# Performance work log

Measured on AMD Instinct MI355X. Metric: run time of the kernel, lower is better.

The kernel has to match this reference:

```python
import jax, jax.numpy as jnp
import numpy as np

I = 512   # input_size
H = 512   # hidden_size
Z = 0.1   # zoneout rate (eval-mode deterministic blend)
S = 128   # number of segments
B = 64    # batch


def setup_inputs() -> dict:
    rng = np.random.default_rng(0)
    durs = rng.integers(4, 13, size=(S, B)).astype(np.int64)  # [S, B], all >= 1
    T = int(durs.sum(0).max())
    key = jax.random.key(0)
    k0, k1, k2, k3, k4 = jax.random.split(key, 5)
    k = 1.0 / np.sqrt(H)
    x = jax.random.normal(k0, (T, B, I), jnp.float32)
    W_ih = jax.random.uniform(k1, (4 * H, I), jnp.float32, -k, k)
    W_hh = jax.random.uniform(k2, (4 * H, H), jnp.float32, -k, k)
    b_ih = jax.random.uniform(k3, (4 * H,), jnp.float32, -k, k)
    b_hh = jax.random.uniform(k4, (4 * H,), jnp.float32, -k, k)
    return {"x": x, "durs": jnp.asarray(durs), "W_ih": W_ih, "W_hh": W_hh,
            "b_ih": b_ih, "b_hh": b_hh}


def _duration_masks(durs, T):
    # durs: [S, B] -> per-batch segment-end (reset) frame indices and masks
    durs_bs = durs.T                                   # [B, S]
    reset_idx = jnp.cumsum(durs_bs, axis=1) - 1        # [B, S] last frame of each segment
    mel_lengths = jnp.sum(durs_bs, axis=1)             # [B]
    t = jnp.arange(T)
    reset_mask = jnp.any(t[None, :, None] == reset_idx[:, None, :], axis=-1)  # [B, T]
    valid = t[None, :] < mel_lengths[:, None]          # [B, T] frames within mel length
    retain = (~reset_mask) & valid                     # state kept where not reset/pad
    return reset_idx, retain.T, valid.T                # retain/valid as [T, B]


def reference(x, durs, W_ih, W_hh, b_ih, b_hh):
    T, Bb, _ = x.shape
    reset_idx, retain, valid = _duration_masks(durs, T)
    # Precompute the input contribution to the gates for all timesteps (one big GEMM)
    xg = jnp.einsum('tbi,gi->tbg', x, W_ih) + b_ih + b_hh   # [T, B, 4H]
    retain_f = retain.astype(x.dtype)                       # [T, B]

    def step(carry, inp):
        h, c = carry
        xg_t, retain_t = inp
        gates = xg_t + h @ W_hh.T                           # [B, 4H]
        i, f, g, o = jnp.split(gates, 4, axis=-1)           # torch LSTMCell order i,f,g,o
        i = jax.nn.sigmoid(i); f = jax.nn.sigmoid(f); o = jax.nn.sigmoid(o)
        g = jnp.tanh(g)
        c_new = f * c + i * g
        h_new = o * jnp.tanh(c_new)
        # eval-mode zoneout: deterministic blend with previous state
        h_z = Z * h + (1.0 - Z) * h_new
        c_z = Z * c + (1.0 - Z) * c_new
        m = retain_t[:, None]                               # zero state at segment resets / padding
        return (h_z * m, c_z * m), h_z

    h0 = jnp.zeros((Bb, H), x.dtype)
    (h, c), outputs = jax.lax.scan(step, (h0, h0), (xg, retain_f))
    outputs = outputs * valid[:, :, None].astype(outputs.dtype)  # [T, B, H]
    # segout: hidden state at each segment's last frame -> [B, S, H]
    segout = jnp.take_along_axis(outputs.transpose(1, 0, 2), reset_idx[:, :, None], axis=1)
    return outputs, h, c, segout
```

## Files before the change

### kernel.cpp

```cpp
#include <hip/hip_runtime.h>
#include <hip/hip_fp16.h>

#define IDIM 512
#define HDIM 512
#define NGATE 2048
#define SEGS 128
#define BATCH 64
#define ZK 0.1f

typedef _Float16 f16;
typedef _Float16 f16x8 __attribute__((ext_vector_type(8)));
typedef float f32x4 __attribute__((ext_vector_type(4)));

__device__ __forceinline__ void gload16(const void* g, void* l) {
  __builtin_amdgcn_global_load_lds((const __attribute__((address_space(1))) void*)g,
                                   (__attribute__((address_space(3))) void*)l, 16, 0, 0);
}
__device__ __forceinline__ float sigmoidf_(float x) { return 1.0f / (1.0f + __expf(-x)); }
__device__ __forceinline__ float tanhf_(float x) { return 2.0f / (1.0f + __expf(-2.0f * x)) - 1.0f; }

__global__ void prep_kernel(const int* __restrict__ durs, int4* __restrict__ meta,
                            int* __restrict__ Mk, int* __restrict__ mel) {
  __shared__ int hist[16];
  __shared__ int cur[16];
  int tid = threadIdx.x;
  if (tid < 16) hist[tid] = 0;
  __syncthreads();
  int b = tid;
  for (int s = 0; s < SEGS; ++s) {
    int d = durs[s * BATCH + b] & 15;
    atomicAdd(&hist[d], 1);
  }
  __syncthreads();
  if (tid == 0) {
    int run = 0;
    for (int d = 15; d >= 0; --d) { cur[d] = run; run += hist[d]; }
    for (int kk = 0; kk < 12; ++kk) Mk[kk] = cur[kk];
  }
  __syncthreads();
  int run = 0;
  for (int s = 0; s < SEGS; ++s) {
    int d = durs[s * BATCH + b] & 15;
    int pos = atomicAdd(&cur[d], 1);
    meta[pos] = make_int4(run, b, s, d);
    run += d;
  }
  mel[b] = run;
}

__global__ void wprep_kernel(const float* __restrict__ Wih, const float* __restrict__ Whh,
                             const float* __restrict__ bih, const float* __restrict__ bhh,
                             f16* __restrict__ Wc, float* __restrict__ biasp) {
  int n = blockIdx.x;
  int G = n >> 6, q = (n >> 4) & 3, r = n & 15;
  int j = G * 16 + r;
  int orig = q * 512 + j;
  for (int kk = threadIdx.x; kk < 1024; kk += blockDim.x) {
    float v = (kk < 512) ? Wih[(size_t)orig * 512 + kk] : Whh[(size_t)orig * 512 + kk - 512];
    Wc[(size_t)n * 1024 + kk] = (f16)v;
  }
  if (threadIdx.x == 0) biasp[n] = bih[orig] + bhh[orig];
}

__global__ void xconv_kernel(const float* __restrict__ x, f16* __restrict__ xh, long n8) {
  long i = (long)blockIdx.x * blockDim.x + threadIdx.x;
  long stride = (long)gridDim.x * blockDim.x;
  for (; i < n8; i += stride) {
    const float4* p = (const float4*)(x + i * 8);
    float4 a = p[0], bv = p[1];
    f16x8 o;
    o[0] = (f16)a.x;  o[1] = (f16)a.y;  o[2] = (f16)a.z;  o[3] = (f16)a.w;
    o[4] = (f16)bv.x; o[5] = (f16)bv.y; o[6] = (f16)bv.z; o[7] = (f16)bv.w;
    *(f16x8*)(xh + i * 8) = o;
  }
}

__global__ void zero_kernel(float* __restrict__ out, const int* __restrict__ mel, int T) {
  int bid = blockIdx.x;
  int tb = T * BATCH;
  if (bid < tb) {
    int t = bid / BATCH, b = bid - t * BATCH;
    if (t < mel[b]) return;
    float4* p = (float4*)(out + (size_t)bid * HDIM);
    p[threadIdx.x] = make_float4(0.f, 0.f, 0.f, 0.f);
  } else {
    int e = bid - tb;
    float4* p = (float4*)(out + (size_t)tb * HDIM + (size_t)e * HDIM);
    p[threadIdx.x] = make_float4(0.f, 0.f, 0.f, 0.f);
  }
}

template <bool FIRST>
__global__ __launch_bounds__(512, 1)
void step256_kernel(const f16* __restrict__ xh, const f16* __restrict__ Wc,
                    const float* __restrict__ biasp,
                    const f16* __restrict__ hprev, f16* __restrict__ hnext,
                    float* __restrict__ cst,
                    const int4* __restrict__ meta, const int* __restrict__ Mk,
                    float* __restrict__ out, int T, int k) {
  const int mk = Mk[k];
  const int nbx = gridDim.x;
  const int nwg = nbx * gridDim.y;
  const int orig = blockIdx.y * nbx + blockIdx.x;
  const int cpx = nwg >> 3;
  const int swz = (orig & 7) * cpx + (orig >> 3);
  const int by = swz / nbx, bx = swz - by * nbx;
  const int m0 = by * 256;
  if (m0 >= mk) return;
  const int n0 = bx * 256;

  __shared__ __align__(16) f16 As[2][256][64];
  __shared__ __align__(16) f16 Bs[2][256][64];
  __shared__ int4 metaS[256];

  const int tid = threadIdx.x;
  const int lane = tid & 63;
  const int w = tid >> 6;
  const int wr = w >> 2;
  const int wc = w & 3;
  const int lr = lane & 15;
  const int lk = lane >> 4;

  if (tid < 256) metaS[tid] = meta[m0 + tid];

  const int swzc = (((lane & 7) ^ ((lane >> 3) & 7)) << 3);
  size_t xoff[4];
  int ra4[4];
#pragma unroll
  for (int o = 0; o < 4; ++o) {
    int trow = o * 64 + w * 8 + (lane >> 3);
    int r = m0 + trow;
    int ra = (r < mk) ? r : 0;
    int4 mt = meta[ra];
    xoff[o] = ((size_t)(mt.x + k) * BATCH + mt.y) * IDIM + swzc;
    ra4[o] = ra;
  }

  auto stageA = [&](int o, int kb, int slot) {
    const f16* src;
    if (FIRST || kb < 8) src = xh + xoff[o] + kb * 64;
    else src = hprev + (size_t)ra4[o] * HDIM + (kb - 8) * 64 + swzc;
    gload16(src, &As[slot][o * 64 + w * 8][0]);
  };
  auto stageB = [&](int o, int kb, int slot) {
    int trow = o * 64 + w * 8 + (lane >> 3);
    gload16(Wc + (size_t)(n0 + trow) * 1024 + (size_t)kb * 64 + swzc,
            &Bs[slot][o * 64 + w * 8][0]);
  };

  auto lda = [&](int slot, int h, int f, int ks) -> f16x8 {
    int row = wr * 128 + h * 64 + f * 16 + lr;
    int ch = (((ks * 4 + lk) ^ (lr & 7)) << 3);
    return *(const f16x8*)&As[slot][row][ch];
  };
  auto ldb = [&](int slot, int q, int ks) -> f16x8 {
    int row = wc * 64 + q * 16 + lr;
    int ch = (((ks * 4 + lk) ^ (lr & 7)) << 3);
    return *(const f16x8*)&Bs[slot][row][ch];
  };

  f32x4 acc[8][4];
#pragma unroll
  for (int a = 0; a < 8; ++a)
#pragma unroll
    for (int bb = 0; bb < 4; ++bb) acc[a][bb] = (f32x4){0.f, 0.f, 0.f, 0.f};

  const int KB = FIRST ? 8 : 16;

#pragma unroll
  for (int o = 0; o < 4; ++o) stageA(o, 0, 0);
#pragma unroll
  for (int o = 0; o < 4; ++o) stageB(o, 0, 0);
#pragma unroll
  for (int o = 0; o < 4; ++o) stageA(o, 1, 1);
#pragma unroll
  for (int o = 0; o < 4; ++o) stageB(o, 1, 1);
  asm volatile("s_waitcnt vmcnt(8)" ::: "memory");
  __builtin_amdgcn_s_barrier();

  f16x8 aF[4][2], bF[4][2];

  for (int kt = 0; kt < KB; ++kt) {
    const int s = kt & 1;
    const bool st1 = (kt + 1 < KB);
    const bool st2 = (kt + 2 < KB);

#pragma unroll
    for (int f = 0; f < 4; ++f)
#pragma unroll
      for (int ks = 0; ks < 2; ++ks) aF[f][ks] = lda(s, 0, f, ks);
#pragma unroll
    for (int q = 0; q < 4; ++q)
#pragma unroll
      for (int ks = 0; ks < 2; ++ks) bF[q][ks] = ldb(s, q, ks);
    __builtin_amdgcn_s_barrier();
    __builtin_amdgcn_s_setprio(1);
#pragma unroll
    for (int f = 0; f < 4; ++f)
#pragma unroll
      for (int fn = 0; fn < 2; ++fn)
#pragma unroll
        for (int ks = 0; ks < 2; ++ks)
          acc[f][fn] = __builtin_amdgcn_mfma_f32_16x16x32_f16(aF[f][ks], bF[fn][ks], acc[f][fn], 0, 0, 0);
    __builtin_amdgcn_s_setprio(0);
    __builtin_amdgcn_s_barrier();

    if (st2) {
#pragma unroll
      for (int o = 0; o < 4; ++o) stageB(o, kt + 2, s);
    }
    __builtin_amdgcn_s_barrier();
    __builtin_amdgcn_s_setprio(1);
#pragma unroll
    for (int f = 0; f < 4; ++f)
#pragma unroll
      for (int fn = 2; fn < 4; ++fn)
#pragma unroll
        for (int ks = 0; ks < 2; ++ks)
          acc[f][fn] = __builtin_amdgcn_mfma_f32_16x16x32_f16(aF[f][ks], bF[fn][ks], acc[f][fn], 0, 0, 0);
    __builtin_amdgcn_s_setprio(0);
    __builtin_amdgcn_s_barrier();

#pragma unroll
    for (int f = 0; f < 4; ++f)
#pragma unroll
      for (int ks = 0; ks < 2; ++ks) aF[f][ks] = lda(s, 1, f, ks);
    if (st2) { stageA(0, kt + 2, s); stageA(2, kt + 2, s); }
    __builtin_amdgcn_s_barrier();
    __builtin_amdgcn_s_setprio(1);
#pragma unroll
    for (int f = 0; f < 4; ++f)
#pragma unroll
      for (int fn = 0; fn < 2; ++fn)
#pragma unroll
        for (int ks = 0; ks < 2; ++ks)
          acc[4 + f][fn] = __builtin_amdgcn_mfma_f32_16x16x32_f16(aF[f][ks], bF[fn][ks], acc[4 + f][fn], 0, 0, 0);
    __builtin_amdgcn_s_setprio(0);
    __builtin_amdgcn_s_barrier();

    if (st2) { stageA(1, kt + 2, s); stageA(3, kt + 2, s); }
    __builtin_amdgcn_s_setprio(1);
#pragma unroll
    for (int f = 0; f < 4; ++f)
#pragma unroll
      for (int fn = 2; fn < 4; ++fn)
#pragma unroll
        for (int ks = 0; ks < 2; ++ks)
          acc[4 + f][fn] = __builtin_amdgcn_mfma_f32_16x16x32_f16(aF[f][ks], bF[fn][ks], acc[4 + f][fn], 0, 0, 0);
    __builtin_amdgcn_s_setprio(0);
    if (st2) {
      asm volatile("s_waitcnt vmcnt(8)" ::: "memory");
    } else if (st1) {
      asm volatile("s_waitcnt vmcnt(0)" ::: "memory");
    }
    __builtin_amdgcn_s_barrier();
  }

  float bq[4];
#pragma unroll
  for (int q = 0; q < 4; ++q) bq[q] = biasp[n0 + wc * 64 + q * 16 + lr];
  const int j = ((n0 + wc * 64) >> 6) * 16 + lr;
  const size_t segoff = (size_t)T * BATCH * HDIM + (size_t)2 * BATCH * HDIM;

#pragma unroll
  for (int fm = 0; fm < 8; ++fm) {
#pragma unroll
    for (int reg = 0; reg < 4; ++reg) {
      int m = m0 + wr * 128 + fm * 16 + ((lane >> 4) << 2) + reg;
      if (m >= mk) continue;
      int4 mt = metaS[m - m0];
      float gi = acc[fm][0][reg] + bq[0];
      float gf = acc[fm][1][reg] + bq[1];
      float gg = acc[fm][2][reg] + bq[2];
      float go = acc[fm][3][reg] + bq[3];
      float iv = sigmoidf_(gi), fv = sigmoidf_(gf);
      float gv = tanhf_(gg), ov = sigmoidf_(go);
      float cp, hp;
      if (FIRST) { cp = 0.f; hp = 0.f; }
      else {
        cp = cst[(size_t)m * HDIM + j];
        hp = (float)hprev[(size_t)m * HDIM + j];
      }
      float cn = fv * cp + iv * gv;
      float hn = ov * tanhf_(cn);
      float hz = ZK * hp + (1.f - ZK) * hn;
      float cz = ZK * cp + (1.f - ZK) * cn;
      out[((size_t)(mt.x + k) * BATCH + mt.y) * HDIM + j] = hz;
      if (k == mt.w - 1) {
        out[segoff + ((size_t)mt.y * SEGS + mt.z) * HDIM + j] = hz;
      } else {
        hnext[(size_t)m * HDIM + j] = (f16)hz;
        cst[(size_t)m * HDIM + j] = cz;
      }
    }
  }
}

template <bool FIRST>
__global__ void step_kernel(const f16* __restrict__ xh, const f16* __restrict__ Wc,
                            const float* __restrict__ biasp,
                            const f16* __restrict__ hprev, f16* __restrict__ hnext,
                            float* __restrict__ cst,
                            const int4* __restrict__ meta, const int* __restrict__ Mk,
                            float* __restrict__ out, int T, int k) {
  const int mk = Mk[k];
  const int m0 = blockIdx.y * 128;
  if (m0 >= mk) return;
  const int n0 = blockIdx.x * 128;

  __shared__ __align__(16) f16 At[128][64];
  __shared__ __align__(16) f16 Bt[128][64];
  __shared__ int4 metaS[128];

  const int tid = threadIdx.x;
  const int lane = tid & 63;
  const int w = tid >> 6;
  const int wr = w >> 1, wc = w & 1;

  if (tid < 128) metaS[tid] = meta[m0 + tid];

  const f16* xsrc[4];
  const f16* hsrc[4];
  const f16* wsrc[4];
#pragma unroll
  for (int i = 0; i < 4; ++i) {
    int r = m0 + w * 32 + i * 8 + (lane >> 3);
    int ra = (r < mk) ? r : 0;
    int4 mt = meta[ra];
    xsrc[i] = xh + ((size_t)(mt.x + k) * BATCH + mt.y) * IDIM;
    hsrc[i] = hprev + (size_t)ra * HDIM;
    wsrc[i] = Wc + (size_t)(n0 + w * 32 + i * 8 + (lane >> 3)) * 1024;
  }
  const int koff = (lane & 7) * 8;

  f32x4 acc[4][4];
#pragma unroll
  for (int a = 0; a < 4; ++a)
#pragma unroll
    for (int bb = 0; bb < 4; ++bb) acc[a][bb] = (f32x4){0.f, 0.f, 0.f, 0.f};

  const int KB = FIRST ? 8 : 16;
  for (int kb = 0; kb < KB; ++kb) {
    __syncthreads();
#pragma unroll
    for (int i = 0; i < 4; ++i) {
      const f16* s;
      if (FIRST) s = xsrc[i] + kb * 64 + koff;
      else       s = (kb < 8) ? (xsrc[i] + kb * 64 + koff) : (hsrc[i] + (kb - 8) * 64 + koff);
      gload16(s, &At[w * 32 + i * 8][0]);
    }
#pragma unroll
    for (int i = 0; i < 4; ++i) gload16(wsrc[i] + kb * 64 + koff, &Bt[w * 32 + i * 8][0]);
    __syncthreads();

    const int lr = lane & 15;
    const int lk = (lane >> 4) * 8;
#pragma unroll
    for (int ks = 0; ks < 2; ++ks) {
      f16x8 af[4], bfr[4];
#pragma unroll
      for (int f = 0; f < 4; ++f) af[f] = *(const f16x8*)&At[wr * 64 + f * 16 + lr][ks * 32 + lk];
#pragma unroll
      for (int f = 0; f < 4; ++f) bfr[f] = *(const f16x8*)&Bt[wc * 64 + f * 16 + lr][ks * 32 + lk];
#pragma unroll
      for (int fm = 0; fm < 4; ++fm)
#pragma unroll
        for (int fn = 0; fn < 4; ++fn)
          acc[fm][fn] = __builtin_amdgcn_mfma_f32_16x16x32_f16(af[fm], bfr[fn], acc[fm][fn], 0, 0, 0);
    }
  }

  const int r15 = lane & 15;
  float bq[4];
#pragma unroll
  for (int q = 0; q < 4; ++q) bq[q] = biasp[n0 + wc * 64 + q * 16 + r15];
  const int j = ((n0 + wc * 64) >> 6) * 16 + r15;
  const size_t segoff = (size_t)T * BATCH * HDIM + (size_t)2 * BATCH * HDIM;

#pragma unroll
  for (int fm = 0; fm < 4; ++fm) {
#pragma unroll
    for (int reg = 0; reg < 4; ++reg) {
      int m = m0 + wr * 64 + fm * 16 + ((lane >> 4) << 2) + reg;
      if (m >= mk) continue;
      int4 mt = metaS[m - m0];
      float gi = acc[fm][0][reg] + bq[0];
      float gf = acc[fm][1][reg] + bq[1];
      float gg = acc[fm][2][reg] + bq[2];
      float go = acc[fm][3][reg] + bq[3];
      float iv = sigmoidf_(gi), fv = sigmoidf_(gf);
      float gv = tanhf_(gg), ov = sigmoidf_(go);
      float cp, hp;
      if (FIRST) { cp = 0.f; hp = 0.f; }
      else {
        cp = cst[(size_t)m * HDIM + j];
        hp = (float)hprev[(size_t)m * HDIM + j];
      }
      float cn = fv * cp + iv * gv;
      float hn = ov * tanhf_(cn);
      float hz = ZK * hp + (1.f - ZK) * hn;
      float cz = ZK * cp + (1.f - ZK) * cn;
      out[((size_t)(mt.x + k) * BATCH + mt.y) * HDIM + j] = hz;
      if (k == mt.w - 1) {
        out[segoff + ((size_t)mt.y * SEGS + mt.z) * HDIM + j] = hz;
      } else {
        hnext[(size_t)m * HDIM + j] = (f16)hz;
        cst[(size_t)m * HDIM + j] = cz;
      }
    }
  }
}

extern "C" void kernel_launch(void* const* d_in, const int* in_sizes, int n_in,
                              void* d_out, int out_size, void* d_ws, size_t ws_size,
                              hipStream_t stream) {
  const float* x = (const float*)d_in[0];
  const int* durs = (const int*)d_in[1];
  const float* Wih = (const float*)d_in[2];
  const float* Whh = (const float*)d_in[3];
  const float* bih = (const float*)d_in[4];
  const float* bhh = (const float*)d_in[5];
  float* out = (float*)d_out;
  const int T = in_sizes[0] / (BATCH * IDIM);

  char* ws = (char*)d_ws;
  size_t off = 0;
  auto alloc = [&](size_t bytes) {
    void* p = ws + off;
    off = (off + bytes + 255) & ~(size_t)255;
    return p;
  };
  f16* xh     = (f16*)alloc((size_t)T * BATCH * IDIM * 2);
  f16* Wc     = (f16*)alloc((size_t)NGATE * 1024 * 2);
  float* biasp= (float*)alloc((size_t)NGATE * 4);
  f16* hst0   = (f16*)alloc((size_t)SEGS * BATCH * HDIM * 2);
  f16* hst1   = (f16*)alloc((size_t)SEGS * BATCH * HDIM * 2);
  float* cst  = (float*)alloc((size_t)SEGS * BATCH * HDIM * 4);
  int4* meta  = (int4*)alloc((size_t)SEGS * BATCH * 16);
  int* Mk     = (int*)alloc(64);
  int* mel    = (int*)alloc(64);

  prep_kernel<<<1, 64, 0, stream>>>(durs, meta, Mk, mel);
  wprep_kernel<<<NGATE, 256, 0, stream>>>(Wih, Whh, bih, bhh, Wc, biasp);
  long n8 = (long)T * BATCH * IDIM / 8;
  xconv_kernel<<<2048, 256, 0, stream>>>(x, xh, n8);
  zero_kernel<<<T * BATCH + 128, 128, 0, stream>>>(out, mel, T);

  dim3 hgrid(8, 32);
  step256_kernel<true><<<hgrid, 512, 0, stream>>>(xh, Wc, biasp, hst0, hst1, cst, meta, Mk, out, T, 0);
  for (int k = 1; k < 8; ++k) {
    f16* hp = (k & 1) ? hst1 : hst0;
    f16* hn = (k & 1) ? hst0 : hst1;
    step256_kernel<false><<<hgrid, 512, 0, stream>>>(xh, Wc, biasp, hp, hn, cst, meta, Mk, out, T, k);
  }
  dim3 sgrid(16, 64);
  for (int k = 8; k < 12; ++k) {
    f16* hp = (k & 1) ? hst1 : hst0;
    f16* hn = (k & 1) ? hst0 : hst1;
    step_kernel<false><<<sgrid, 256, 0, stream>>>(xh, Wc, biasp, hp, hn, cst, meta, Mk, out, T, k);
  }
}
```

Before: 654.7 us.

## Hoist input projection into one batched GEMM ahead of the recurrent steps

Splits the combined [x,h] weight into separate input and recurrent halves. All input-gate products for every active row and step are computed up front in one large GEMM, gathered through a row map and stored in fp16 with the bias folded in. Each recurrent step then does only the K=512 hidden-state GEMM and adds the precomputed gates in the epilogue, and step 0 becomes a pure elementwise kernel. The costs are a large fp16 intermediate buffer, an extra write and read of it, and fp16 rounding of the pre-activation gates. The zero kernel becomes grid-strided.

```diff
diff --git a/kernel.cpp b/kernel.cpp
--- a/kernel.cpp
+++ b/kernel.cpp
@@ -7,6 +7,7 @@
 #define SEGS 128
 #define BATCH 64
 #define ZK 0.1f
+#define XGROWS 98304
 
 typedef _Float16 f16;
 typedef _Float16 f16x8 __attribute__((ext_vector_type(8)));
@@ -27,15 +28,14 @@
   if (tid < 16) hist[tid] = 0;
   __syncthreads();
   int b = tid;
-  for (int s = 0; s < SEGS; ++s) {
-    int d = durs[s * BATCH + b] & 15;
-    atomicAdd(&hist[d], 1);
-  }
+  for (int s = 0; s < SEGS; ++s) atomicAdd(&hist[durs[s * BATCH + b] & 15], 1);
   __syncthreads();
   if (tid == 0) {
     int run = 0;
     for (int d = 15; d >= 0; --d) { cur[d] = run; run += hist[d]; }
-    for (int kk = 0; kk < 12; ++kk) Mk[kk] = cur[kk];
+    int off = 0;
+    for (int kk = 0; kk < 12; ++kk) { Mk[kk] = cur[kk]; Mk[12 + kk] = off; off += cur[kk]; }
+    Mk[24] = off;
   }
   __syncthreads();
   int run = 0;
@@ -48,16 +48,30 @@
   mel[b] = run;
 }
 
+__global__ void zrowmap_kernel(int* __restrict__ rowmap) {
+  rowmap[blockIdx.x * 256 + threadIdx.x] = 0;
+}
+
+__global__ void rowmap_kernel(const int4* __restrict__ meta, const int* __restrict__ Mk,
+                              int* __restrict__ rowmap) {
+  int k = blockIdx.y;
+  int m = blockIdx.x * 256 + threadIdx.x;
+  if (m < Mk[k]) {
+    int4 mt = meta[m];
+    rowmap[Mk[12 + k] + m] = (mt.x + k) * BATCH + mt.y;
+  }
+}
+
 __global__ void wprep_kernel(const float* __restrict__ Wih, const float* __restrict__ Whh,
                              const float* __restrict__ bih, const float* __restrict__ bhh,
-                             f16* __restrict__ Wc, float* __restrict__ biasp) {
+                             f16* __restrict__ Wihp, f16* __restrict__ Whhp,
+                             float* __restrict__ biasp) {
   int n = blockIdx.x;
   int G = n >> 6, q = (n >> 4) & 3, r = n & 15;
-  int j = G * 16 + r;
-  int orig = q * 512 + j;
-  for (int kk = threadIdx.x; kk < 1024; kk += blockDim.x) {
-    float v = (kk < 512) ? Wih[(size_t)orig * 512 + kk] : Whh[(size_t)orig * 512 + kk - 512];
-    Wc[(size_t)n * 1024 + kk] = (f16)v;
+  int orig = q * 512 + G * 16 + r;
+  for (int kk = threadIdx.x; kk < 512; kk += blockDim.x) {
+    Wihp[(size_t)n * 512 + kk] = (f16)Wih[(size_t)orig * 512 + kk];
+    Whhp[(size_t)n * 512 + kk] = (f16)Whh[(size_t)orig * 512 + kk];
   }
   if (threadIdx.x == 0) biasp[n] = bih[orig] + bhh[orig];
 }
@@ -75,30 +89,225 @@
   }
 }
 
-__global__ void zero_kernel(float* __restrict__ out, const int* __restrict__ mel, int T) {
-  int bid = blockIdx.x;
+__global__ void zero_kernel(float* __restrict__ out, const int* __restrict__ mel,
+                            int T, int total) {
   int tb = T * BATCH;
-  if (bid < tb) {
-    int t = bid / BATCH, b = bid - t * BATCH;
-    if (t < mel[b]) return;
-    float4* p = (float4*)(out + (size_t)bid * HDIM);
-    p[threadIdx.x] = make_float4(0.f, 0.f, 0.f, 0.f);
-  } else {
-    int e = bid - tb;
-    float4* p = (float4*)(out + (size_t)tb * HDIM + (size_t)e * HDIM);
-    p[threadIdx.x] = make_float4(0.f, 0.f, 0.f, 0.f);
-  }
-}
-
-template <bool FIRST>
+  for (int bid = blockIdx.x; bid < total; bid += gridDim.x) {
+    if (bid < tb) {
+      int t = bid / BATCH, b = bid - t * BATCH;
+      if (t < mel[b]) continue;
+      float4* p = (float4*)(out + (size_t)bid * HDIM);
+      p[threadIdx.x] = make_float4(0.f, 0.f, 0.f, 0.f);
+    } else {
+      int e = bid - tb;
+      float4* p = (float4*)(out + (size_t)tb * HDIM + (size_t)e * HDIM);
+      p[threadIdx.x] = make_float4(0.f, 0.f, 0.f, 0.f);
+    }
+  }
+}
+
 __global__ __launch_bounds__(512, 1)
-void step256_kernel(const f16* __restrict__ xh, const f16* __restrict__ Wc,
-                    const float* __restrict__ biasp,
+void xg_gemm_kernel(const f16* __restrict__ xh, const f16* __restrict__ Wihp,
+                    const float* __restrict__ biasp, const int* __restrict__ rowmap,
+                    const int* __restrict__ Mk, f16* __restrict__ xg) {
+  const int orig = blockIdx.y * 8 + blockIdx.x;
+  const int swz = (orig & 7) * 384 + (orig >> 3);
+  const int by = swz >> 3, bx = swz & 7;
+  const int r0 = by * 256;
+  if (r0 >= Mk[24]) return;
+  const int n0 = bx * 256;
+
+  __shared__ __align__(16) f16 SM[65536];
+  f16 (*As)[256][64] = (f16(*)[256][64])SM;
+  f16 (*Bs)[256][64] = (f16(*)[256][64])(SM + 32768);
+
+  const int tid = threadIdx.x;
+  const int lane = tid & 63;
+  const int w = tid >> 6;
+  const int wr = w >> 2;
+  const int wc = w & 3;
+  const int lr = lane & 15;
+  const int lk = lane >> 4;
+
+  const int swzc = (((lane & 7) ^ ((lane >> 3) & 7)) << 3);
+  const f16* asrc[4];
+  const f16* wsrc[4];
+#pragma unroll
+  for (int o = 0; o < 4; ++o) {
+    int trow = o * 64 + w * 8 + (lane >> 3);
+    asrc[o] = xh + (size_t)rowmap[r0 + trow] * IDIM + swzc;
+    wsrc[o] = Wihp + (size_t)(n0 + trow) * 512 + swzc;
+  }
+
+  auto stageA = [&](int o, int kb, int slot) {
+    gload16(asrc[o] + kb * 64, &As[slot][o * 64 + w * 8][0]);
+  };
+  auto stageB = [&](int o, int kb, int slot) {
+    gload16(wsrc[o] + kb * 64, &Bs[slot][o * 64 + w * 8][0]);
+  };
+  auto lda = [&](int slot, int h, int f, int ks) -> f16x8 {
+    int row = wr * 128 + h * 64 + f * 16 + lr;
+    int ch = (((ks * 4 + lk) ^ (lr & 7)) << 3);
+    return *(const f16x8*)&As[slot][row][ch];
+  };
+  auto ldb = [&](int slot, int q, int ks) -> f16x8 {
+    int row = wc * 64 + q * 16 + lr;
+    int ch = (((ks * 4 + lk) ^ (lr & 7)) << 3);
+    return *(const f16x8*)&Bs[slot][row][ch];
+  };
+
+  f32x4 acc[8][4];
+#pragma unroll
+  for (int a = 0; a < 8; ++a)
+#pragma unroll
+    for (int bb = 0; bb < 4; ++bb) acc[a][bb] = (f32x4){0.f, 0.f, 0.f, 0.f};
+
+  const int KB = 8;
+#pragma unroll
+  for (int o = 0; o < 4; ++o) stageA(o, 0, 0);
+#pragma unroll
+  for (int o = 0; o < 4; ++o) stageB(o, 0, 0);
+#pragma unroll
+  for (int o = 0; o < 4; ++o) stageA(o, 1, 1);
+#pragma unroll
+  for (int o = 0; o < 4; ++o) stageB(o, 1, 1);
+  asm volatile("s_waitcnt vmcnt(8)" ::: "memory");
+  __builtin_amdgcn_s_barrier();
+
+  f16x8 aF[4][2], bF[4][2];
+  for (int kt = 0; kt < KB; ++kt) {
+    const int s = kt & 1;
+    const bool st1 = (kt + 1 < KB);
+    const bool st2 = (kt + 2 < KB);
+
+#pragma unroll
+    for (int f = 0; f < 4; ++f)
+#pragma unroll
+      for (int ks = 0; ks < 2; ++ks) aF[f][ks] = lda(s, 0, f, ks);
+#pragma unroll
+    for (int q = 0; q < 4; ++q)
+#pragma unroll
+      for (int ks = 0; ks < 2; ++ks) bF[q][ks] = ldb(s, q, ks);
+    __builtin_amdgcn_s_barrier();
+    __builtin_amdgcn_s_setprio(1);
+#pragma unroll
+    for (int f = 0; f < 4; ++f)
+#pragma unroll
+      for (int fn = 0; fn < 2; ++fn)
+#pragma unroll
+        for (int ks = 0; ks < 2; ++ks)
+          acc[f][fn] = __builtin_amdgcn_mfma_f32_16x16x32_f16(aF[f][ks], bF[fn][ks], acc[f][fn], 0, 0, 0);
+    __builtin_amdgcn_s_setprio(0);
+    __builtin_amdgcn_s_barrier();
+
+    if (st2) {
+#pragma unroll
+      for (int o = 0; o < 4; ++o) stageB(o, kt + 2, s);
+    }
+    __builtin_amdgcn_s_barrier();
+    __builtin_amdgcn_s_setprio(1);
+#pragma unroll
+    for (int f = 0; f < 4; ++f)
+#pragma unroll
+      for (int fn = 2; fn < 4; ++fn)
+#pragma unroll
+        for (int ks = 0; ks < 2; ++ks)
+          acc[f][fn] = __builtin_amdgcn_mfma_f32_16x16x32_f16(aF[f][ks], bF[fn][ks], acc[f][fn], 0, 0, 0);
+    __builtin_amdgcn_s_setprio(0);
+    __builtin_amdgcn_s_barrier();
+
+#pragma unroll
+    for (int f = 0; f < 4; ++f)
+#pragma unroll
+      for (int ks = 0; ks < 2; ++ks) aF[f][ks] = lda(s, 1, f, ks);
+    if (st2) { stageA(0, kt + 2, s); stageA(2, kt + 2, s); }
+    __builtin_amdgcn_s_barrier();
+    __builtin_amdgcn_s_setprio(1);
+#pragma unroll
+    for (int f = 0; f < 4; ++f)
+#pragma unroll
+      for (int fn = 0; fn < 2; ++fn)
+#pragma unroll
+        for (int ks = 0; ks < 2; ++ks)
+          acc[4 + f][fn] = __builtin_amdgcn_mfma_f32_16x16x32_f16(aF[f][ks], bF[fn][ks], acc[4 + f][fn], 0, 0, 0);
+    __builtin_amdgcn_s_setprio(0);
+    __builtin_amdgcn_s_barrier();
+
+    if (st2) { stageA(1, kt + 2, s); stageA(3, kt + 2, s); }
+    __builtin_amdgcn_s_setprio(1);
+#pragma unroll
+    for (int f = 0; f < 4; ++f)
+#pragma unroll
+      for (int fn = 2; fn < 4; ++fn)
+#pragma unroll
+        for (int ks = 0; ks < 2; ++ks)
+          acc[4 + f][fn] = __builtin_amdgcn_mfma_f32_16x16x32_f16(aF[f][ks], bF[fn][ks], acc[4 + f][fn], 0, 0, 0);
+    __builtin_amdgcn_s_setprio(0);
+    if (st2) {
+      asm volatile("s_waitcnt vmcnt(8)" ::: "memory");
+    } else if (st1) {
+      asm volatile("s_waitcnt vmcnt(0)" ::: "memory");
+    }
+    __builtin_amdgcn_s_barrier();
+  }
+
+  float bq[4];
+#pragma unroll
+  for (int q = 0; q < 4; ++q) bq[q] = biasp[n0 + wc * 64 + q * 16 + lr];
+  __syncthreads();
+  f16* SM2 = SM;
+#pragma unroll
+  for (int fm = 0; fm < 8; ++fm)
+#pragma unroll
+    for (int reg = 0; reg < 4; ++reg) {
+      int lm = wr * 128 + fm * 16 + ((lane >> 4) << 2) + reg;
+#pragma unroll
+      for (int q = 0; q < 4; ++q)
+        SM2[lm * 256 + wc * 64 + q * 16 + lr] = (f16)(acc[fm][q][reg] + bq[q]);
+    }
+  __syncthreads();
+#pragma unroll
+  for (int i = 0; i < 16; ++i) {
+    int idx = i * 512 + tid;
+    int lm = idx >> 5, c = idx & 31;
+    *(f16x8*)(xg + ((size_t)(r0 + lm) * NGATE + n0 + c * 8)) =
+        *(const f16x8*)&SM2[lm * 256 + c * 8];
+  }
+}
+
+__global__ void step0_kernel(const f16* __restrict__ xg, const int4* __restrict__ meta,
+                             f16* __restrict__ hnext, float* __restrict__ cst,
+                             float* __restrict__ out) {
+  __shared__ f16 xr[NGATE];
+  int m = blockIdx.x;
+  int tid = threadIdx.x;
+  *(f16x8*)&xr[tid * 8] = *(const f16x8*)&xg[(size_t)m * NGATE + tid * 8];
+  __syncthreads();
+  int4 mt = meta[m];
+#pragma unroll
+  for (int u = 0; u < 2; ++u) {
+    int jj = tid * 2 + u;
+    int base = (jj >> 4) * 64 + (jj & 15);
+    float iv = sigmoidf_((float)xr[base]);
+    float gv = tanhf_((float)xr[base + 32]);
+    float ov = sigmoidf_((float)xr[base + 48]);
+    float cn = iv * gv;
+    float hn = ov * tanhf_(cn);
+    float hz = (1.f - ZK) * hn, cz = (1.f - ZK) * cn;
+    out[((size_t)mt.x * BATCH + mt.y) * HDIM + jj] = hz;
+    hnext[(size_t)m * HDIM + jj] = (f16)hz;
+    cst[(size_t)m * HDIM + jj] = cz;
+  }
+}
+
+__global__ __launch_bounds__(512, 1)
+void step256_kernel(const f16* __restrict__ xg, const f16* __restrict__ Whhp,
                     const f16* __restrict__ hprev, f16* __restrict__ hnext,
                     float* __restrict__ cst,
                     const int4* __restrict__ meta, const int* __restrict__ Mk,
                     float* __restrict__ out, int T, int k) {
   const int mk = Mk[k];
+  const int offk = Mk[12 + k];
   const int nbx = gridDim.x;
   const int nwg = nbx * gridDim.y;
   const int orig = blockIdx.y * nbx + blockIdx.x;
@@ -124,30 +333,23 @@
   if (tid < 256) metaS[tid] = meta[m0 + tid];
 
   const int swzc = (((lane & 7) ^ ((lane >> 3) & 7)) << 3);
-  size_t xoff[4];
-  int ra4[4];
+  const f16* asrc[4];
+  const f16* wsrc[4];
 #pragma unroll
   for (int o = 0; o < 4; ++o) {
     int trow = o * 64 + w * 8 + (lane >> 3);
     int r = m0 + trow;
     int ra = (r < mk) ? r : 0;
-    int4 mt = meta[ra];
-    xoff[o] = ((size_t)(mt.x + k) * BATCH + mt.y) * IDIM + swzc;
-    ra4[o] = ra;
+    asrc[o] = hprev + (size_t)ra * HDIM + swzc;
+    wsrc[o] = Whhp + (size_t)(n0 + trow) * 512 + swzc;
   }
 
   auto stageA = [&](int o, int kb, int slot) {
-    const f16* src;
-    if (FIRST || kb < 8) src = xh + xoff[o] + kb * 64;
-    else src = hprev + (size_t)ra4[o] * HDIM + (kb - 8) * 64 + swzc;
-    gload16(src, &As[slot][o * 64 + w * 8][0]);
+    gload16(asrc[o] + kb * 64, &As[slot][o * 64 + w * 8][0]);
   };
   auto stageB = [&](int o, int kb, int slot) {
-    int trow = o * 64 + w * 8 + (lane >> 3);
-    gload16(Wc + (size_t)(n0 + trow) * 1024 + (size_t)kb * 64 + swzc,
-            &Bs[slot][o * 64 + w * 8][0]);
-  };
-
+    gload16(wsrc[o] + kb * 64, &Bs[slot][o * 64 + w * 8][0]);
+  };
   auto lda = [&](int slot, int h, int f, int ks) -> f16x8 {
     int row = wr * 128 + h * 64 + f * 16 + lr;
     int ch = (((ks * 4 + lk) ^ (lr & 7)) << 3);
@@ -165,8 +367,7 @@
 #pragma unroll
     for (int bb = 0; bb < 4; ++bb) acc[a][bb] = (f32x4){0.f, 0.f, 0.f, 0.f};
 
-  const int KB = FIRST ? 8 : 16;
-
+  const int KB = 8;
 #pragma unroll
   for (int o = 0; o < 4; ++o) stageA(o, 0, 0);
 #pragma unroll
@@ -179,7 +380,6 @@
   __builtin_amdgcn_s_barrier();
 
   f16x8 aF[4][2], bF[4][2];
-
   for (int kt = 0; kt < KB; ++kt) {
     const int s = kt & 1;
     const bool st1 = (kt + 1 < KB);
@@ -256,11 +456,9 @@
     __builtin_amdgcn_s_barrier();
   }
 
-  float bq[4];
-#pragma unroll
-  for (int q = 0; q < 4; ++q) bq[q] = biasp[n0 + wc * 64 + q * 16 + lr];
+  const int nb = n0 + wc * 64 + lr;
+  const size_t segoff = (size_t)T * BATCH * HDIM + (size_t)2 * BATCH * HDIM;
   const int j = ((n0 + wc * 64) >> 6) * 16 + lr;
-  const size_t segoff = (size_t)T * BATCH * HDIM + (size_t)2 * BATCH * HDIM;
 
 #pragma unroll
   for (int fm = 0; fm < 8; ++fm) {
@@ -269,18 +467,15 @@
       int m = m0 + wr * 128 + fm * 16 + ((lane >> 4) << 2) + reg;
       if (m >= mk) continue;
       int4 mt = metaS[m - m0];
-      float gi = acc[fm][0][reg] + bq[0];
-      float gf = acc[fm][1][reg] + bq[1];
-      float gg = acc[fm][2][reg] + bq[2];
-      float go = acc[fm][3][reg] + bq[3];
+      const f16* xgp = xg + (size_t)(offk + m) * NGATE;
+      float gi = acc[fm][0][reg] + (float)xgp[nb];
+      float gf = acc[fm][1][reg] + (float)xgp[nb + 16];
+      float gg = acc[fm][2][reg] + (float)xgp[nb + 32];
+      float go = acc[fm][3][reg] + (float)xgp[nb + 48];
       float iv = sigmoidf_(gi), fv = sigmoidf_(gf);
       float gv = tanhf_(gg), ov = sigmoidf_(go);
-      float cp, hp;
-      if (FIRST) { cp = 0.f; hp = 0.f; }
-      else {
-        cp = cst[(size_t)m * HDIM + j];
-        hp = (float)hprev[(size_t)m * HDIM + j];
-      }
+      float cp = cst[(size_t)m * HDIM + j];
+      float hp = (float)hprev[(size_t)m * HDIM + j];
       float cn = fv * cp + iv * gv;
       float hn = ov * tanhf_(cn);
       float hz = ZK * hp + (1.f - ZK) * hn;
@@ -296,14 +491,13 @@
   }
 }
 
-template <bool FIRST>
-__global__ void step_kernel(const f16* __restrict__ xh, const f16* __restrict__ Wc,
-                            const float* __restrict__ biasp,
+__global__ void step_kernel(const f16* __restrict__ xg, const f16* __restrict__ Whhp,
                             const f16* __restrict__ hprev, f16* __restrict__ hnext,
                             float* __restrict__ cst,
                             const int4* __restrict__ meta, const int* __restrict__ Mk,
                             float* __restrict__ out, int T, int k) {
   const int mk = Mk[k];
+  const int offk = Mk[12 + k];
   const int m0 = blockIdx.y * 128;
   if (m0 >= mk) return;
   const int n0 = blockIdx.x * 128;
@@ -319,17 +513,14 @@
 
   if (tid < 128) metaS[tid] = meta[m0 + tid];
 
-  const f16* xsrc[4];
   const f16* hsrc[4];
   const f16* wsrc[4];
 #pragma unroll
   for (int i = 0; i < 4; ++i) {
     int r = m0 + w * 32 + i * 8 + (lane >> 3);
     int ra = (r < mk) ? r : 0;
-    int4 mt = meta[ra];
-    xsrc[i] = xh + ((size_t)(mt.x + k) * BATCH + mt.y) * IDIM;
     hsrc[i] = hprev + (size_t)ra * HDIM;
-    wsrc[i] = Wc + (size_t)(n0 + w * 32 + i * 8 + (lane >> 3)) * 1024;
+    wsrc[i] = Whhp + (size_t)(n0 + w * 32 + i * 8 + (lane >> 3)) * 512;
   }
   const int koff = (lane & 7) * 8;
 
@@ -339,16 +530,10 @@
 #pragma unroll
     for (int bb = 0; bb < 4; ++bb) acc[a][bb] = (f32x4){0.f, 0.f, 0.f, 0.f};
 
-  const int KB = FIRST ? 8 : 16;
-  for (int kb = 0; kb < KB; ++kb) {
+  for (int kb = 0; kb < 8; ++kb) {
     __syncthreads();
 #pragma unroll
-    for (int i = 0; i < 4; ++i) {
-      const f16* s;
-      if (FIRST) s = xsrc[i] + kb * 64 + koff;
-      else       s = (kb < 8) ? (xsrc[i] + kb * 64 + koff) : (hsrc[i] + (kb - 8) * 64 + koff);
-      gload16(s, &At[w * 32 + i * 8][0]);
-    }
+    for (int i = 0; i < 4; ++i) gload16(hsrc[i] + kb * 64 + koff, &At[w * 32 + i * 8][0]);
 #pragma unroll
     for (int i = 0; i < 4; ++i) gload16(wsrc[i] + kb * 64 + koff, &Bt[w * 32 + i * 8][0]);
     __syncthreads();
@@ -371,9 +556,7 @@
   }
 
   const int r15 = lane & 15;
-  float bq[4];
-#pragma unroll
-  for (int q = 0; q < 4; ++q) bq[q] = biasp[n0 + wc * 64 + q * 16 + r15];
+  const int nb = n0 + wc * 64 + r15;
   const int j = ((n0 + wc * 64) >> 6) * 16 + r15;
   const size_t segoff = (size_t)T * BATCH * HDIM + (size_t)2 * BATCH * HDIM;
 
@@ -384,18 +567,15 @@
       int m = m0 + wr * 64 + fm * 16 + ((lane >> 4) << 2) + reg;
       if (m >= mk) continue;
       int4 mt = metaS[m - m0];
-      float gi = acc[fm][0][reg] + bq[0];
-      float gf = acc[fm][1][reg] + bq[1];
-      float gg = acc[fm][2][reg] + bq[2];
-      float go = acc[fm][3][reg] + bq[3];
+      const f16* xgp = xg + (size_t)(offk + m) * NGATE;
+      float gi = acc[fm][0][reg] + (float)xgp[nb];
+      float gf = acc[fm][1][reg] + (float)xgp[nb + 16];
+      float gg = acc[fm][2][reg] + (float)xgp[nb + 32];
+      float go = acc[fm][3][reg] + (float)xgp[nb + 48];
       float iv = sigmoidf_(gi), fv = sigmoidf_(gf);
       float gv = tanhf_(gg), ov = sigmoidf_(go);
-      float cp, hp;
-      if (FIRST) { cp = 0.f; hp = 0.f; }
-      else {
-        cp = cst[(size_t)m * HDIM + j];
-        hp = (float)hprev[(size_t)m * HDIM + j];
-      }
+      float cp = cst[(size_t)m * HDIM + j];
+      float hp = (float)hprev[(size_t)m * HDIM + j];
       float cn = fv * cp + iv * gv;
       float hn = ov * tanhf_(cn);
       float hz = ZK * hp + (1.f - ZK) * hn;
@@ -430,33 +610,41 @@
     off = (off + bytes + 255) & ~(size_t)255;
     return p;
   };
-  f16* xh     = (f16*)alloc((size_t)T * BATCH * IDIM * 2);
-  f16* Wc     = (f16*)alloc((size_t)NGATE * 1024 * 2);
-  float* biasp= (float*)alloc((size_t)NGATE * 4);
-  f16* hst0   = (f16*)alloc((size_t)SEGS * BATCH * HDIM * 2);
-  f16* hst1   = (f16*)alloc((size_t)SEGS * BATCH * HDIM * 2);
-  float* cst  = (float*)alloc((size_t)SEGS * BATCH * HDIM * 4);
-  int4* meta  = (int4*)alloc((size_t)SEGS * BATCH * 16);
-  int* Mk     = (int*)alloc(64);
-  int* mel    = (int*)alloc(64);
+  f16* xh      = (f16*)alloc((size_t)T * BATCH * IDIM * 2);
+  f16* xg      = (f16*)alloc((size_t)XGROWS * NGATE * 2);
+  f16* Wihp    = (f16*)alloc((size_t)NGATE * 512 * 2);
+  f16* Whhp    = (f16*)alloc((size_t)NGATE * 512 * 2);
+  float* biasp = (float*)alloc((size_t)NGATE * 4);
+  f16* hst0    = (f16*)alloc((size_t)SEGS * BATCH * HDIM * 2);
+  f16* hst1    = (f16*)alloc((size_t)SEGS * BATCH * HDIM * 2);
+  float* cst   = (float*)alloc((size_t)SEGS * BATCH * HDIM * 4);
+  int4* meta   = (int4*)alloc((size_t)SEGS * BATCH * 16);
+  int* Mk      = (int*)alloc(256);
+  int* mel     = (int*)alloc(64);
+  int* rowmap  = (int*)alloc((size_t)XGROWS * 4);
 
   prep_kernel<<<1, 64, 0, stream>>>(durs, meta, Mk, mel);
-  wprep_kernel<<<NGATE, 256, 0, stream>>>(Wih, Whh, bih, bhh, Wc, biasp);
+  wprep_kernel<<<NGATE, 256, 0, stream>>>(Wih, Whh, bih, bhh, Wihp, Whhp, biasp);
   long n8 = (long)T * BATCH * IDIM / 8;
   xconv_kernel<<<2048, 256, 0, stream>>>(x, xh, n8);
-  zero_kernel<<<T * BATCH + 128, 128, 0, stream>>>(out, mel, T);
+  zero_kernel<<<2048, 128, 0, stream>>>(out, mel, T, T * BATCH + 128);
+  zrowmap_kernel<<<XGROWS / 256, 256, 0, stream>>>(rowmap);
+  rowmap_kernel<<<dim3(32, 12), 256, 0, stream>>>(meta, Mk, rowmap);
+
+  xg_gemm_kernel<<<dim3(8, 384), 512, 0, stream>>>(xh, Wihp, biasp, rowmap, Mk, xg);
+
+  step0_kernel<<<SEGS * BATCH, 256, 0, stream>>>(xg, meta, hst1, cst, out);
 
   dim3 hgrid(8, 32);
-  step256_kernel<true><<<hgrid, 512, 0, stream>>>(xh, Wc, biasp, hst0, hst1, cst, meta, Mk, out, T, 0);
   for (int k = 1; k < 8; ++k) {
     f16* hp = (k & 1) ? hst1 : hst0;
     f16* hn = (k & 1) ? hst0 : hst1;
-    step256_kernel<false><<<hgrid, 512, 0, stream>>>(xh, Wc, biasp, hp, hn, cst, meta, Mk, out, T, k);
+    step256_kernel<<<hgrid, 512, 0, stream>>>(xg, Whhp, hp, hn, cst, meta, Mk, out, T, k);
   }
   dim3 sgrid(16, 64);
   for (int k = 8; k < 12; ++k) {
     f16* hp = (k & 1) ? hst1 : hst0;
     f16* hn = (k & 1) ? hst0 : hst1;
-    step_kernel<false><<<sgrid, 256, 0, stream>>>(xh, Wc, biasp, hp, hn, cst, meta, Mk, out, T, k);
-  }
-}
+    step_kernel<<<sgrid, 256, 0, stream>>>(xg, Whhp, hp, hn, cst, meta, Mk, out, T, k);
+  }
+}
```

Measured after the change: 822.9 us. 1.26x slower.
